# Performance work log

Hardware: AMD Instinct MI355X
Metric: run time of the kernel (lower is better)

Reference implementation:

```python
import jax, jax.numpy as jnp
import numpy as np

MIN_NORM = 1e-15
N = 10000        # num_nodes
E = 320000       # num edges (avg degree 32)
F_IN = 512       # in_features
HID = 256        # hardcoded encoder hidden dim
D_HYP = 2        # Poincare embedding dim
HEIGHT = 2
MAX_SIZE = 0.999
MIN_SCALE = HEIGHT * (MAX_SIZE / (HEIGHT + 1))  # = 0.666, scale clamp lower bound
MAX_SCALE = MAX_SIZE


def setup_inputs() -> dict:
    key = jax.random.key(0)
    ks = jax.random.split(key, 5)
    feature = jax.random.normal(ks[0], (N, F_IN), jnp.float32)
    edge_index = jax.random.randint(ks[1], (2, E), 0, N, dtype=jnp.int64)
    W1 = jax.random.normal(ks[2], (F_IN, HID), jnp.float32) / np.sqrt(F_IN).astype(np.float32)
    b1 = jnp.zeros((HID,), jnp.float32)
    W2 = jax.random.normal(ks[3], (HID, D_HYP), jnp.float32) / np.sqrt(HID).astype(np.float32)
    b2 = jnp.zeros((D_HYP,), jnp.float32)
    scale = jnp.ones((1,), jnp.float32)  # init_size overridden to 1.0 in __init__
    return {"feature": feature, "edge_index": edge_index, "W1": W1, "b1": b1,
            "W2": W2, "b2": b2, "scale": scale}


def _gcn_agg(h, src, dst):
    # symmetric-normalized edge_index gather/aggregate (message passing)
    deg = jax.ops.segment_sum(jnp.ones((src.shape[0],), h.dtype), dst, num_segments=N)
    deg = jnp.maximum(deg, 1.0)
    norm = jax.lax.rsqrt(deg[src] * deg[dst])            # [E]
    msg = h[src] * norm[:, None]                          # [E, C] gather (irregular)
    return jax.ops.segment_sum(msg, dst, num_segments=N)  # [N, C] scatter-add


def reference(feature, edge_index, W1, b1, W2, b2, scale):
    src, dst = edge_index[0], edge_index[1]
    # 2-layer graph encoder (linear -> aggregate -> relu, linear -> aggregate)
    h = jax.nn.relu(_gcn_agg(feature @ W1 + b1, src, dst))   # [N, HID]
    u = _gcn_agg(h @ W2 + b2, src, dst)                      # [N, D_HYP] tangent at origin
    # lift to Lorentz model (k=-1) via expmap0: x = [cosh|u|, sinh|u| * u/|u|]
    un = jnp.maximum(jnp.linalg.norm(u, axis=-1, keepdims=True), MIN_NORM)
    x_l = jnp.concatenate([jnp.cosh(un), jnp.sinh(un) * u / un], axis=-1)  # [N, D_HYP+1]
    # Lorentz -> Poincare: p = x_space / (1 + x_time)
    p = x_l[:, 1:] / (1.0 + x_l[:, :1])
    # normalize: F.normalize(p, dim=-1) * scale.clamp(min_size, max_size)
    pn = jnp.maximum(jnp.linalg.norm(p, axis=-1, keepdims=True), 1e-12)
    s = jnp.clip(scale, MIN_SCALE, MAX_SCALE)
    p = p / pn * s
    # project onto Poincare ball of curvature k=-1 with eps=MIN_NORM
    norm = jnp.maximum(jnp.linalg.norm(p, axis=-1, keepdims=True), MIN_NORM)
    maxnorm = 1.0 - MIN_NORM
    return jnp.where(norm > maxnorm, p / norm * maxnorm, p)
```

## Files before the change

### kernel.cpp

```cpp
#include <hip/hip_runtime.h>
#include <math.h>

#define N_NODES 10000
#define N_EDGES 320000
#define F_IN 512
#define HID 256
#define PAD_DEG 80
#define LDSTR 40
#define N_TILES (157 * 4)
#define BUILD_BLKS ((N_EDGES + 255) / 256)

typedef _Float16 half8 __attribute__((ext_vector_type(8)));
typedef float floatx4 __attribute__((ext_vector_type(4)));

__device__ __forceinline__ void fma4(float4& acc, float s, const float4& v) {
    acc.x += s * v.x; acc.y += s * v.y; acc.z += s * v.z; acc.w += s * v.w;
}


__global__ __launch_bounds__(256) void k_pre(const float* __restrict__ W1,
                                             int* __restrict__ count,
                                             _Float16* __restrict__ Bt_hi,
                                             _Float16* __restrict__ Bt_lo) {
    int i = blockIdx.x * blockDim.x + threadIdx.x;
    if (i < 10240) count[i] = 0;
    int k = i >> 8, n = i & 255;
    float v = W1[i];
    _Float16 hi = (_Float16)v;
    Bt_hi[n * F_IN + k] = hi;
    Bt_lo[n * F_IN + k] = (_Float16)(v - (float)hi);
}


__global__ __launch_bounds__(256) void k_combo(const float* __restrict__ A,
                                               const _Float16* __restrict__ Bt_hi,
                                               const _Float16* __restrict__ Bt_lo,
                                               const float* __restrict__ b1,
                                               float* __restrict__ h0,
                                               const int* __restrict__ ei,
                                               int* __restrict__ count,
                                               int* __restrict__ csr) {
    __shared__ _Float16 As_hi[64 * LDSTR], As_lo[64 * LDSTR];
    __shared__ _Float16 Bs_hi[64 * LDSTR], Bs_lo[64 * LDSTR];
    const int tid = threadIdx.x;

    if (blockIdx.x >= N_TILES) {
        int e = (blockIdx.x - N_TILES) * 256 + tid;
        if (e < N_EDGES) {
            int src = ei[e];
            int dst = ei[N_EDGES + e];
            int pos = atomicAdd(&count[dst], 1);
            csr[dst * PAD_DEG + pos] = src;
        }
        return;
    }

    const int lane = tid & 63, w = tid >> 6;
    const int wm = (w >> 1) * 32, wn = (w & 1) * 32;
    const int quad = lane >> 4, l15 = lane & 15;
    const int r = tid >> 2, c = (tid & 3) << 3;
    const int t = blockIdx.x;
    const int row0 = (t >> 2) * 64, col0 = (t & 3) * 64;
    floatx4 acc[2][2] = {};

    for (int k0 = 0; k0 < F_IN; k0 += 32) {
        float av[8];
        int arow = row0 + r;
        if (arow < N_NODES) {
            float4 v0 = *(const float4*)(A + (size_t)arow * F_IN + k0 + c);
            float4 v1 = *(const float4*)(A + (size_t)arow * F_IN + k0 + c + 4);
            av[0] = v0.x; av[1] = v0.y; av[2] = v0.z; av[3] = v0.w;
            av[4] = v1.x; av[5] = v1.y; av[6] = v1.z; av[7] = v1.w;
        } else {
            #pragma unroll
            for (int i = 0; i < 8; ++i) av[i] = 0.f;
        }
        half8 hhi, hlo;
        #pragma unroll
        for (int i = 0; i < 8; ++i) {
            _Float16 h = (_Float16)av[i];
            hhi[i] = h;
            hlo[i] = (_Float16)(av[i] - (float)h);
        }
        *(half8*)&As_hi[r * LDSTR + c] = hhi;
        *(half8*)&As_lo[r * LDSTR + c] = hlo;
        *(half8*)&Bs_hi[r * LDSTR + c] = *(const half8*)(Bt_hi + (size_t)(col0 + r) * F_IN + k0 + c);
        *(half8*)&Bs_lo[r * LDSTR + c] = *(const half8*)(Bt_lo + (size_t)(col0 + r) * F_IN + k0 + c);
        __syncthreads();
        half8 a_hi[2], a_lo[2], b_hi[2], b_lo[2];
        #pragma unroll
        for (int mi = 0; mi < 2; ++mi) {
            int mr = wm + mi * 16 + l15;
            a_hi[mi] = *(half8*)&As_hi[mr * LDSTR + quad * 8];
            a_lo[mi] = *(half8*)&As_lo[mr * LDSTR + quad * 8];
        }
        #pragma unroll
        for (int ni = 0; ni < 2; ++ni) {
            int nr = wn + ni * 16 + l15;
            b_hi[ni] = *(half8*)&Bs_hi[nr * LDSTR + quad * 8];
            b_lo[ni] = *(half8*)&Bs_lo[nr * LDSTR + quad * 8];
        }
        #pragma unroll
        for (int mi = 0; mi < 2; ++mi)
            #pragma unroll
            for (int ni = 0; ni < 2; ++ni) {
                acc[mi][ni] = __builtin_amdgcn_mfma_f32_16x16x32_f16(a_hi[mi], b_hi[ni], acc[mi][ni], 0, 0, 0);
                acc[mi][ni] = __builtin_amdgcn_mfma_f32_16x16x32_f16(a_hi[mi], b_lo[ni], acc[mi][ni], 0, 0, 0);
                acc[mi][ni] = __builtin_amdgcn_mfma_f32_16x16x32_f16(a_lo[mi], b_hi[ni], acc[mi][ni], 0, 0, 0);
            }
        __syncthreads();
    }
    #pragma unroll
    for (int mi = 0; mi < 2; ++mi)
        #pragma unroll
        for (int ni = 0; ni < 2; ++ni) {
            int colb = col0 + wn + ni * 16 + l15;
            float bias = b1[colb];
            #pragma unroll
            for (int reg = 0; reg < 4; ++reg) {
                int rowb = row0 + wm + mi * 16 + quad * 4 + reg;
                if (rowb < N_NODES) h0[(size_t)rowb * HID + colb] = acc[mi][ni][reg] + bias;
            }
        }
}


__global__ __launch_bounds__(256) void k_agg1(const float* __restrict__ h0,
                                              const int* __restrict__ csr,
                                              const int* __restrict__ count,
                                              const float* __restrict__ W2,
                                              const float* __restrict__ b2,
                                              float* __restrict__ u0) {
    int n = blockIdx.x * 4 + (threadIdx.x >> 6);
    int lane = threadIdx.x & 63;
    if (n >= N_NODES) return;
    int deg = count[n];
    float degd = (float)(deg > 0 ? deg : 1);
    const int* row = csr + (size_t)n * PAD_DEG;
    int off = lane << 2;
    float4 acc0 = {0,0,0,0}, acc1 = {0,0,0,0}, acc2 = {0,0,0,0}, acc3 = {0,0,0,0};
    int j = 0;
    for (; j + 8 <= deg; j += 8) {
        int s0 = row[j+0], s1 = row[j+1], s2 = row[j+2], s3 = row[j+3];
        int s4 = row[j+4], s5 = row[j+5], s6 = row[j+6], s7 = row[j+7];
        int c0 = count[s0], c1 = count[s1], c2 = count[s2], c3 = count[s3];
        int c4 = count[s4], c5 = count[s5], c6 = count[s6], c7 = count[s7];
        float4 v0 = *(const float4*)(h0 + (size_t)s0 * HID + off);
        float4 v1 = *(const float4*)(h0 + (size_t)s1 * HID + off);
        float4 v2 = *(const float4*)(h0 + (size_t)s2 * HID + off);
        float4 v3 = *(const float4*)(h0 + (size_t)s3 * HID + off);
        float4 v4 = *(const float4*)(h0 + (size_t)s4 * HID + off);
        float4 v5 = *(const float4*)(h0 + (size_t)s5 * HID + off);
        float4 v6 = *(const float4*)(h0 + (size_t)s6 * HID + off);
        float4 v7 = *(const float4*)(h0 + (size_t)s7 * HID + off);
        fma4(acc0, rsqrtf((float)(c0 > 0 ? c0 : 1) * degd), v0);
        fma4(acc1, rsqrtf((float)(c1 > 0 ? c1 : 1) * degd), v1);
        fma4(acc2, rsqrtf((float)(c2 > 0 ? c2 : 1) * degd), v2);
        fma4(acc3, rsqrtf((float)(c3 > 0 ? c3 : 1) * degd), v3);
        fma4(acc0, rsqrtf((float)(c4 > 0 ? c4 : 1) * degd), v4);
        fma4(acc1, rsqrtf((float)(c5 > 0 ? c5 : 1) * degd), v5);
        fma4(acc2, rsqrtf((float)(c6 > 0 ? c6 : 1) * degd), v6);
        fma4(acc3, rsqrtf((float)(c7 > 0 ? c7 : 1) * degd), v7);
    }
    for (; j < deg; ++j) {
        int s = row[j];
        int cs = count[s];
        float4 v = *(const float4*)(h0 + (size_t)s * HID + off);
        fma4(acc0, rsqrtf((float)(cs > 0 ? cs : 1) * degd), v);
    }
    acc0.x += acc1.x + acc2.x + acc3.x;
    acc0.y += acc1.y + acc2.y + acc3.y;
    acc0.z += acc1.z + acc2.z + acc3.z;
    acc0.w += acc1.w + acc2.w + acc3.w;
    acc0.x = fmaxf(acc0.x, 0.f); acc0.y = fmaxf(acc0.y, 0.f);
    acc0.z = fmaxf(acc0.z, 0.f); acc0.w = fmaxf(acc0.w, 0.f);
    float4 wa = *(const float4*)(W2 + (lane << 3));
    float4 wb = *(const float4*)(W2 + (lane << 3) + 4);
    float p0 = acc0.x * wa.x + acc0.y * wa.z + acc0.z * wb.x + acc0.w * wb.z;
    float p1 = acc0.x * wa.y + acc0.y * wa.w + acc0.z * wb.y + acc0.w * wb.w;
    #pragma unroll
    for (int o = 32; o > 0; o >>= 1) {
        p0 += __shfl_down(p0, o);
        p1 += __shfl_down(p1, o);
    }
    if (lane == 0) {
        u0[2 * n]     = p0 + b2[0];
        u0[2 * n + 1] = p1 + b2[1];
    }
}


__global__ __launch_bounds__(256) void k_agg2(const float* __restrict__ u0,
                                              const int* __restrict__ csr,
                                              const int* __restrict__ count,
                                              const float* __restrict__ scale,
                                              float* __restrict__ out) {
    int n = blockIdx.x * 4 + (threadIdx.x >> 6);
    int lane = threadIdx.x & 63;
    if (n >= N_NODES) return;
    int deg = count[n];
    float degd = (float)(deg > 0 ? deg : 1);
    const int* row = csr + (size_t)n * PAD_DEG;
    float a0 = 0.f, a1 = 0.f;
    for (int j = lane; j < deg; j += 64) {
        int s = row[j];
        int cs = count[s];
        float wq = rsqrtf((float)(cs > 0 ? cs : 1) * degd);
        float2 uv = *(const float2*)(u0 + 2 * (size_t)s);
        a0 += wq * uv.x;
        a1 += wq * uv.y;
    }
    #pragma unroll
    for (int o = 32; o > 0; o >>= 1) {
        a0 += __shfl_down(a0, o);
        a1 += __shfl_down(a1, o);
    }
    if (lane == 0) {
        float un = fmaxf(sqrtf(a0 * a0 + a1 * a1), 1e-15f);
        float t = tanhf(0.5f * un) / un;
        float p0 = a0 * t, p1 = a1 * t;
        float pn = fmaxf(sqrtf(p0 * p0 + p1 * p1), 1e-12f);
        float s = fminf(fmaxf(scale[0], 0.666f), 0.999f);
        p0 = p0 / pn * s; p1 = p1 / pn * s;
        float nn = fmaxf(sqrtf(p0 * p0 + p1 * p1), 1e-15f);
        if (nn > 1.0f) { p0 = p0 / nn; p1 = p1 / nn; }
        out[2 * n]     = p0;
        out[2 * n + 1] = p1;
    }
}


extern "C" void kernel_launch(void* const* d_in, const int* in_sizes, int n_in,
                              void* d_out, int out_size, void* d_ws, size_t ws_size,
                              hipStream_t stream) {
    const float* feature = (const float*)d_in[0];
    const int*   ei      = (const int*)d_in[1];
    const float* W1      = (const float*)d_in[2];
    const float* b1      = (const float*)d_in[3];
    const float* W2      = (const float*)d_in[4];
    const float* b2      = (const float*)d_in[5];
    const float* scale   = (const float*)d_in[6];
    float* out = (float*)d_out;

    char* W = (char*)d_ws;
    int*      count = (int*)W;
    int*      csr   = (int*)(W + 40960);
    float*    h0    = (float*)(W + 3240960);
    float*    u0    = (float*)(W + 13480960);
    _Float16* Bt_hi = (_Float16*)(W + 13560960);
    _Float16* Bt_lo = (_Float16*)(W + 13823104);

    k_pre<<<dim3(512), dim3(256), 0, stream>>>(W1, count, Bt_hi, Bt_lo);
    k_combo<<<dim3(N_TILES + BUILD_BLKS), dim3(256), 0, stream>>>(
        feature, Bt_hi, Bt_lo, b1, h0, ei, count, csr);
    k_agg1<<<dim3((N_NODES + 3) / 4), dim3(256), 0, stream>>>(h0, csr, count, W2, b2, u0);
    k_agg2<<<dim3((N_NODES + 3) / 4), dim3(256), 0, stream>>>(u0, csr, count, scale, out);
}
```

Measured before the change: 153.3 us.

## Enlarge GEMM tiles to 128x128 and stage neighbor weights in LDS

```diff
diff --git a/kernel.cpp b/kernel.cpp
--- a/kernel.cpp
+++ b/kernel.cpp
@@ -7,7 +7,7 @@
 #define HID 256
 #define PAD_DEG 80
 #define LDSTR 40
-#define N_TILES (157 * 4)
+#define N_GTILES 158
 #define BUILD_BLKS ((N_EDGES + 255) / 256)
 
 typedef _Float16 half8 __attribute__((ext_vector_type(8)));
@@ -40,12 +40,12 @@
                                                const int* __restrict__ ei,
                                                int* __restrict__ count,
                                                int* __restrict__ csr) {
-    __shared__ _Float16 As_hi[64 * LDSTR], As_lo[64 * LDSTR];
-    __shared__ _Float16 Bs_hi[64 * LDSTR], Bs_lo[64 * LDSTR];
+    __shared__ _Float16 As_hi[128 * LDSTR], As_lo[128 * LDSTR];
+    __shared__ _Float16 Bs_hi[128 * LDSTR], Bs_lo[128 * LDSTR];
     const int tid = threadIdx.x;
 
-    if (blockIdx.x >= N_TILES) {
-        int e = (blockIdx.x - N_TILES) * 256 + tid;
+    if (blockIdx.x >= N_GTILES) {
+        int e = (blockIdx.x - N_GTILES) * 256 + tid;
         if (e < N_EDGES) {
             int src = ei[e];
             int dst = ei[N_EDGES + e];
@@ -56,64 +56,72 @@
     }
 
     const int lane = tid & 63, w = tid >> 6;
-    const int wm = (w >> 1) * 32, wn = (w & 1) * 32;
+    const int wm = (w >> 1) * 64, wn = (w & 1) * 64;
     const int quad = lane >> 4, l15 = lane & 15;
-    const int r = tid >> 2, c = (tid & 3) << 3;
+    const int r = tid >> 1, c = (tid & 1) << 4;
     const int t = blockIdx.x;
-    const int row0 = (t >> 2) * 64, col0 = (t & 3) * 64;
-    floatx4 acc[2][2] = {};
+    const int row0 = (t >> 1) * 128, col0 = (t & 1) * 128;
+    floatx4 acc[4][4] = {};
+
+    const int arow = row0 + r;
+    const float* Aptr = A + (size_t)arow * F_IN + c;
+    const _Float16* Bh = Bt_hi + (size_t)(col0 + r) * F_IN + c;
+    const _Float16* Bl = Bt_lo + (size_t)(col0 + r) * F_IN + c;
 
     for (int k0 = 0; k0 < F_IN; k0 += 32) {
-        float av[8];
-        int arow = row0 + r;
+        float av[16];
         if (arow < N_NODES) {
-            float4 v0 = *(const float4*)(A + (size_t)arow * F_IN + k0 + c);
-            float4 v1 = *(const float4*)(A + (size_t)arow * F_IN + k0 + c + 4);
-            av[0] = v0.x; av[1] = v0.y; av[2] = v0.z; av[3] = v0.w;
-            av[4] = v1.x; av[5] = v1.y; av[6] = v1.z; av[7] = v1.w;
+            #pragma unroll
+            for (int q = 0; q < 4; ++q) {
+                float4 v = *(const float4*)(Aptr + k0 + q * 4);
+                av[q * 4 + 0] = v.x; av[q * 4 + 1] = v.y;
+                av[q * 4 + 2] = v.z; av[q * 4 + 3] = v.w;
+            }
         } else {
             #pragma unroll
-            for (int i = 0; i < 8; ++i) av[i] = 0.f;
-        }
-        half8 hhi, hlo;
-        #pragma unroll
-        for (int i = 0; i < 8; ++i) {
+            for (int i = 0; i < 16; ++i) av[i] = 0.f;
+        }
+        half8 hhi[2], hlo[2];
+        #pragma unroll
+        for (int i = 0; i < 16; ++i) {
             _Float16 h = (_Float16)av[i];
-            hhi[i] = h;
-            hlo[i] = (_Float16)(av[i] - (float)h);
-        }
-        *(half8*)&As_hi[r * LDSTR + c] = hhi;
-        *(half8*)&As_lo[r * LDSTR + c] = hlo;
-        *(half8*)&Bs_hi[r * LDSTR + c] = *(const half8*)(Bt_hi + (size_t)(col0 + r) * F_IN + k0 + c);
-        *(half8*)&Bs_lo[r * LDSTR + c] = *(const half8*)(Bt_lo + (size_t)(col0 + r) * F_IN + k0 + c);
+            hhi[i >> 3][i & 7] = h;
+            hlo[i >> 3][i & 7] = (_Float16)(av[i] - (float)h);
+        }
+        *(half8*)&As_hi[r * LDSTR + c]     = hhi[0];
+        *(half8*)&As_hi[r * LDSTR + c + 8] = hhi[1];
+        *(half8*)&As_lo[r * LDSTR + c]     = hlo[0];
+        *(half8*)&As_lo[r * LDSTR + c + 8] = hlo[1];
+        *(half8*)&Bs_hi[r * LDSTR + c]     = *(const half8*)(Bh + k0);
+        *(half8*)&Bs_hi[r * LDSTR + c + 8] = *(const half8*)(Bh + k0 + 8);
+        *(half8*)&Bs_lo[r * LDSTR + c]     = *(const half8*)(Bl + k0);
+        *(half8*)&Bs_lo[r * LDSTR + c + 8] = *(const half8*)(Bl + k0 + 8);
         __syncthreads();
-        half8 a_hi[2], a_lo[2], b_hi[2], b_lo[2];
-        #pragma unroll
-        for (int mi = 0; mi < 2; ++mi) {
+        half8 a_hi[4], a_lo[4];
+        #pragma unroll
+        for (int mi = 0; mi < 4; ++mi) {
             int mr = wm + mi * 16 + l15;
             a_hi[mi] = *(half8*)&As_hi[mr * LDSTR + quad * 8];
             a_lo[mi] = *(half8*)&As_lo[mr * LDSTR + quad * 8];
         }
         #pragma unroll
-        for (int ni = 0; ni < 2; ++ni) {
+        for (int ni = 0; ni < 4; ++ni) {
             int nr = wn + ni * 16 + l15;
-            b_hi[ni] = *(half8*)&Bs_hi[nr * LDSTR + quad * 8];
-            b_lo[ni] = *(half8*)&Bs_lo[nr * LDSTR + quad * 8];
-        }
-        #pragma unroll
-        for (int mi = 0; mi < 2; ++mi)
-            #pragma unroll
-            for (int ni = 0; ni < 2; ++ni) {
-                acc[mi][ni] = __builtin_amdgcn_mfma_f32_16x16x32_f16(a_hi[mi], b_hi[ni], acc[mi][ni], 0, 0, 0);
-                acc[mi][ni] = __builtin_amdgcn_mfma_f32_16x16x32_f16(a_hi[mi], b_lo[ni], acc[mi][ni], 0, 0, 0);
-                acc[mi][ni] = __builtin_amdgcn_mfma_f32_16x16x32_f16(a_lo[mi], b_hi[ni], acc[mi][ni], 0, 0, 0);
+            half8 b_hi = *(half8*)&Bs_hi[nr * LDSTR + quad * 8];
+            half8 b_lo = *(half8*)&Bs_lo[nr * LDSTR + quad * 8];
+            #pragma unroll
+            for (int mi = 0; mi < 4; ++mi) {
+                acc[mi][ni] = __builtin_amdgcn_mfma_f32_16x16x32_f16(a_hi[mi], b_hi, acc[mi][ni], 0, 0, 0);
+                acc[mi][ni] = __builtin_amdgcn_mfma_f32_16x16x32_f16(a_hi[mi], b_lo, acc[mi][ni], 0, 0, 0);
+                acc[mi][ni] = __builtin_amdgcn_mfma_f32_16x16x32_f16(a_lo[mi], b_hi, acc[mi][ni], 0, 0, 0);
             }
+        }
         __syncthreads();
     }
     #pragma unroll
-    for (int mi = 0; mi < 2; ++mi)
-        #pragma unroll
-        for (int ni = 0; ni < 2; ++ni) {
+    for (int mi = 0; mi < 4; ++mi)
+        #pragma unroll
+        for (int ni = 0; ni < 4; ++ni) {
             int colb = col0 + wn + ni * 16 + l15;
             float bias = b1[colb];
             #pragma unroll
@@ -131,42 +139,48 @@
                                               const float* __restrict__ W2,
                                               const float* __restrict__ b2,
                                               float* __restrict__ u0) {
-    int n = blockIdx.x * 4 + (threadIdx.x >> 6);
-    int lane = threadIdx.x & 63;
-    if (n >= N_NODES) return;
-    int deg = count[n];
-    float degd = (float)(deg > 0 ? deg : 1);
+    __shared__ int2 nb[4][PAD_DEG];
+    const int wid = threadIdx.x >> 6;
+    const int lane = threadIdx.x & 63;
+    const int n = blockIdx.x * 4 + wid;
+    const int deg = count[n];
+    const float degd = (float)(deg > 0 ? deg : 1);
     const int* row = csr + (size_t)n * PAD_DEG;
-    int off = lane << 2;
+    for (int j = lane; j < deg; j += 64) {
+        int s = row[j];
+        int cs = count[s];
+        float wq = rsqrtf((float)(cs > 0 ? cs : 1) * degd);
+        nb[wid][j] = make_int2(s, __float_as_int(wq));
+    }
+    __syncthreads();
+
+    const int off = lane << 2;
     float4 acc0 = {0,0,0,0}, acc1 = {0,0,0,0}, acc2 = {0,0,0,0}, acc3 = {0,0,0,0};
     int j = 0;
     for (; j + 8 <= deg; j += 8) {
-        int s0 = row[j+0], s1 = row[j+1], s2 = row[j+2], s3 = row[j+3];
-        int s4 = row[j+4], s5 = row[j+5], s6 = row[j+6], s7 = row[j+7];
-        int c0 = count[s0], c1 = count[s1], c2 = count[s2], c3 = count[s3];
-        int c4 = count[s4], c5 = count[s5], c6 = count[s6], c7 = count[s7];
-        float4 v0 = *(const float4*)(h0 + (size_t)s0 * HID + off);
-        float4 v1 = *(const float4*)(h0 + (size_t)s1 * HID + off);
-        float4 v2 = *(const float4*)(h0 + (size_t)s2 * HID + off);
-        float4 v3 = *(const float4*)(h0 + (size_t)s3 * HID + off);
-        float4 v4 = *(const float4*)(h0 + (size_t)s4 * HID + off);
-        float4 v5 = *(const float4*)(h0 + (size_t)s5 * HID + off);
-        float4 v6 = *(const float4*)(h0 + (size_t)s6 * HID + off);
-        float4 v7 = *(const float4*)(h0 + (size_t)s7 * HID + off);
-        fma4(acc0, rsqrtf((float)(c0 > 0 ? c0 : 1) * degd), v0);
-        fma4(acc1, rsqrtf((float)(c1 > 0 ? c1 : 1) * degd), v1);
-        fma4(acc2, rsqrtf((float)(c2 > 0 ? c2 : 1) * degd), v2);
-        fma4(acc3, rsqrtf((float)(c3 > 0 ? c3 : 1) * degd), v3);
-        fma4(acc0, rsqrtf((float)(c4 > 0 ? c4 : 1) * degd), v4);
-        fma4(acc1, rsqrtf((float)(c5 > 0 ? c5 : 1) * degd), v5);
-        fma4(acc2, rsqrtf((float)(c6 > 0 ? c6 : 1) * degd), v6);
-        fma4(acc3, rsqrtf((float)(c7 > 0 ? c7 : 1) * degd), v7);
+        int2 e0 = nb[wid][j+0], e1 = nb[wid][j+1], e2 = nb[wid][j+2], e3 = nb[wid][j+3];
+        int2 e4 = nb[wid][j+4], e5 = nb[wid][j+5], e6 = nb[wid][j+6], e7 = nb[wid][j+7];
+        float4 v0 = *(const float4*)(h0 + ((size_t)e0.x << 8) + off);
+        float4 v1 = *(const float4*)(h0 + ((size_t)e1.x << 8) + off);
+        float4 v2 = *(const float4*)(h0 + ((size_t)e2.x << 8) + off);
+        float4 v3 = *(const float4*)(h0 + ((size_t)e3.x << 8) + off);
+        float4 v4 = *(const float4*)(h0 + ((size_t)e4.x << 8) + off);
+        float4 v5 = *(const float4*)(h0 + ((size_t)e5.x << 8) + off);
+        float4 v6 = *(const float4*)(h0 + ((size_t)e6.x << 8) + off);
+        float4 v7 = *(const float4*)(h0 + ((size_t)e7.x << 8) + off);
+        fma4(acc0, __int_as_float(e0.y), v0);
+        fma4(acc1, __int_as_float(e1.y), v1);
+        fma4(acc2, __int_as_float(e2.y), v2);
+        fma4(acc3, __int_as_float(e3.y), v3);
+        fma4(acc0, __int_as_float(e4.y), v4);
+        fma4(acc1, __int_as_float(e5.y), v5);
+        fma4(acc2, __int_as_float(e6.y), v6);
+        fma4(acc3, __int_as_float(e7.y), v7);
     }
     for (; j < deg; ++j) {
-        int s = row[j];
-        int cs = count[s];
-        float4 v = *(const float4*)(h0 + (size_t)s * HID + off);
-        fma4(acc0, rsqrtf((float)(cs > 0 ? cs : 1) * degd), v);
+        int2 e = nb[wid][j];
+        float4 v = *(const float4*)(h0 + ((size_t)e.x << 8) + off);
+        fma4(acc0, __int_as_float(e.y), v);
     }
     acc0.x += acc1.x + acc2.x + acc3.x;
     acc0.y += acc1.y + acc2.y + acc3.y;
@@ -251,7 +265,7 @@
     _Float16* Bt_lo = (_Float16*)(W + 13823104);
 
     k_pre<<<dim3(512), dim3(256), 0, stream>>>(W1, count, Bt_hi, Bt_lo);
-    k_combo<<<dim3(N_TILES + BUILD_BLKS), dim3(256), 0, stream>>>(
+    k_combo<<<dim3(N_GTILES + BUILD_BLKS), dim3(256), 0, stream>>>(
         feature, Bt_hi, Bt_lo, b1, h0, ei, count, csr);
     k_agg1<<<dim3((N_NODES + 3) / 4), dim3(256), 0, stream>>>(h0, csr, count, W2, b2, u0);
     k_agg2<<<dim3((N_NODES + 3) / 4), dim3(256), 0, stream>>>(u0, csr, count, scale, out);
```

Result: slower. 160.1 us (+4.5%).
